# Kernel optimization log

Measured on AMD Instinct MI355X. Metric: run time of the kernel, lower is better.

The kernel has to match this reference:

```python
import jax, jax.numpy as jnp
import numpy as np

B = 4194304  # number of sequential rows


def setup_inputs() -> dict:
    key = jax.random.key(0)
    k1, k2, k3, k4 = jax.random.split(key, 4)
    x = jax.random.normal(k1, (B, 1, 3), dtype=jnp.float32)
    # nn.Linear(3, 3) params
    lim = 1.0 / np.sqrt(3.0)
    W = jax.random.uniform(k2, (3, 3), minval=-lim, maxval=lim, dtype=jnp.float32)
    b = jax.random.uniform(k3, (3,), minval=-lim, maxval=lim, dtype=jnp.float32)
    # FastNetwork init: (-1-1)*rand([3,1]) + 1  -> uniform in [-1, 1]
    net0 = jax.random.uniform(k4, (3, 1), minval=-1.0, maxval=1.0, dtype=jnp.float32)
    return {"x": x, "W": W, "b": b, "net0": net0}


def reference(x, W, b, net0):
    # x: [B,1,3]; W: [3,3]; b: [3]; net0: [3,1]
    xi = x[:, 0, :]                      # [B,3]
    # Updater: per-row Linear(3,3) -- batched as one matmul
    updates = xi @ W.T + b               # [B,3]

    def step(net, inp):
        x_row, u = inp                   # x_row: [3], u: [3]
        # 1/(1+exp(-10*(net + update - 0.5))) == sigmoid(10*(net + update - 0.5))
        net = jax.nn.sigmoid(10.0 * (net + u[:, None] - 0.5))  # [3,1]
        pred = x_row @ net               # [1]
        return net, pred

    _, preds = jax.lax.scan(step, net0, (xi, updates))
    return preds                         # [B,1]
```

## Files before the change

### kernel.cpp

```cpp
#include <hip/hip_runtime.h>


#if __has_builtin(__builtin_amdgcn_exp2f)
#define EXP2F(v) __builtin_amdgcn_exp2f(v)
#else
#define EXP2F(v) __expf(0.6931471805599453f * (v))
#endif

namespace {
constexpr int   BTOT   = 4194304;
constexpr int   CHUNK  = 16;
constexpr int   BLOCK  = 256;
constexpr int   BSTEPS = BLOCK * CHUNK;
constexpr int   WARM   = 32;
constexpr int   GRID   = BTOT / BSTEPS;
constexpr int   LDSF   = (BSTEPS + WARM) * 3;
constexpr float KEXP   = -14.426950408889634f;
constexpr float EPS    = 1e-6f;
}

#define CVALS(X0, X1, X2)                                                     \
  const float c0 = fmaf(kw00, (X0), fmaf(kw01, (X1), fmaf(kw02, (X2), kb0)));  \
  const float c1 = fmaf(kw10, (X0), fmaf(kw11, (X1), fmaf(kw12, (X2), kb1)));  \
  const float c2 = fmaf(kw20, (X0), fmaf(kw21, (X1), fmaf(kw22, (X2), kb2)));

#define SIG(N, C) __builtin_amdgcn_rcpf(1.0f + EXP2F(fmaf(KEXP, (N), (C))))

#define US(X0, X1, X2)                                                        \
  do {                                                                        \
    CVALS(X0, X1, X2)                                                         \
    lo0 = SIG(lo0, c0); hi0 = SIG(hi0, c0);                                   \
    lo1 = SIG(lo1, c1); hi1 = SIG(hi1, c1);                                   \
    lo2 = SIG(lo2, c2); hi2 = SIG(hi2, c2);                                   \
  } while (0)

#define SS(X0, X1, X2)                                                        \
  do {                                                                        \
    CVALS(X0, X1, X2)                                                         \
    m0 = SIG(m0, c0); m1 = SIG(m1, c1); m2 = SIG(m2, c2);                     \
  } while (0)

#define MS(IDX, X0, X1, X2)                                                   \
  do {                                                                        \
    CVALS(X0, X1, X2)                                                         \
    m0 = SIG(m0, c0); m1 = SIG(m1, c1); m2 = SIG(m2, c2);                     \
    pr[(IDX)] = fmaf((X0), m0, fmaf((X1), m1, (X2) * m2));                    \
  } while (0)

__global__ __launch_bounds__(BLOCK) void Updater_65395172049297_kernel(
    const float* __restrict__ x, const float* __restrict__ W,
    const float* __restrict__ bv, const float* __restrict__ n0v,
    float* __restrict__ out)
{
    __shared__ float lds[LDSF];

    const float kw00 = KEXP * W[0], kw01 = KEXP * W[1], kw02 = KEXP * W[2];
    const float kw10 = KEXP * W[3], kw11 = KEXP * W[4], kw12 = KEXP * W[5];
    const float kw20 = KEXP * W[6], kw21 = KEXP * W[7], kw22 = KEXP * W[8];
    const float kb0 = KEXP * (bv[0] - 0.5f);
    const float kb1 = KEXP * (bv[1] - 0.5f);
    const float kb2 = KEXP * (bv[2] - 0.5f);
    const float n00 = n0v[0], n01 = n0v[1], n02 = n0v[2];

    const long S = (long)blockIdx.x * BSTEPS;
    if (blockIdx.x == 0) {
        const float4* src = reinterpret_cast<const float4*>(x);
        float4*       dst = reinterpret_cast<float4*>(lds + WARM * 3);
        for (int i = threadIdx.x; i < BSTEPS * 3 / 4; i += BLOCK) dst[i] = src[i];
    } else {
        const float4* src = reinterpret_cast<const float4*>(x + 3 * (S - WARM));
        float4*       dst = reinterpret_cast<float4*>(lds);
        for (int i = threadIdx.x; i < LDSF / 4; i += BLOCK) dst[i] = src[i];
    }
    __syncthreads();

    const int  t     = threadIdx.x;
    const long start = S + (long)t * CHUNK;
    const int  wl    = (int)((start < (long)WARM) ? start : (long)WARM);
    const bool exact = (start - wl) == 0;
    const int  gw    = wl >> 2;
    const int  lbeg  = (int)(start - S + WARM) * 3 - wl * 3;

    float lo0, lo1, lo2, hi0, hi1, hi2, m0, m1, m2;
    bool  conv = false;
    int   g    = 0;

    if (exact) {
        m0 = n00; m1 = n01; m2 = n02; conv = true;
    } else {
        lo0 = lo1 = lo2 = 0.0f; hi0 = hi1 = hi2 = 1.0f;
        for (; g < gw; ) {
            const float4* p = reinterpret_cast<const float4*>(&lds[lbeg + 12 * g]);
            const float4 a = p[0], b4 = p[1], c4 = p[2];
            US(a.x, a.y, a.z);
            US(a.w, b4.x, b4.y);
            US(b4.z, b4.w, c4.x);
            US(c4.y, c4.z, c4.w);
            ++g;
            conv = ((hi0 - lo0) < EPS) & ((hi1 - lo1) < EPS) & ((hi2 - lo2) < EPS);
            if (__all(conv)) break;
        }
        if (conv) { m0 = 0.5f * (lo0 + hi0); m1 = 0.5f * (lo1 + hi1); m2 = 0.5f * (lo2 + hi2); }
    }

    if (conv) {
        for (; g < gw; ++g) {
            const float4* p = reinterpret_cast<const float4*>(&lds[lbeg + 12 * g]);
            const float4 a = p[0], b4 = p[1], c4 = p[2];
            SS(a.x, a.y, a.z);
            SS(a.w, b4.x, b4.y);
            SS(b4.z, b4.w, c4.x);
            SS(c4.y, c4.z, c4.w);
        }
    } else {
        for (int a = 1; a < 10 && !conv; ++a) {
            long wl2 = (long)WARM << (2 * a);
            long bgn = start - wl2;
            bool ex2 = (bgn <= 0);
            if (ex2) bgn = 0;
            if (ex2) { lo0 = hi0 = n00; lo1 = hi1 = n01; lo2 = hi2 = n02; }
            else     { lo0 = lo1 = lo2 = 0.0f; hi0 = hi1 = hi2 = 1.0f; }
            for (long s2 = bgn; s2 < start; ++s2) {
                const float X0 = x[3 * s2], X1 = x[3 * s2 + 1], X2 = x[3 * s2 + 2];
                US(X0, X1, X2);
            }
            conv = ex2 || (((hi0 - lo0) < EPS) & ((hi1 - lo1) < EPS) & ((hi2 - lo2) < EPS));
        }
        m0 = 0.5f * (lo0 + hi0); m1 = 0.5f * (lo1 + hi1); m2 = 0.5f * (lo2 + hi2);
    }

    const int lm = (int)(start - S + WARM) * 3;
    float pr[CHUNK];
#pragma unroll
    for (int q = 0; q < CHUNK / 4; ++q) {
        const float4* p = reinterpret_cast<const float4*>(&lds[lm + 12 * q]);
        const float4 a = p[0], b4 = p[1], c4 = p[2];
        MS(4 * q + 0, a.x, a.y, a.z);
        MS(4 * q + 1, a.w, b4.x, b4.y);
        MS(4 * q + 2, b4.z, b4.w, c4.x);
        MS(4 * q + 3, c4.y, c4.z, c4.w);
    }

    float4* op = reinterpret_cast<float4*>(out + start);
#pragma unroll
    for (int i = 0; i < CHUNK / 4; ++i)
        op[i] = make_float4(pr[4 * i + 0], pr[4 * i + 1], pr[4 * i + 2], pr[4 * i + 3]);
}

extern "C" void kernel_launch(void* const* d_in, const int* in_sizes, int n_in,
                              void* d_out, int out_size, void* d_ws, size_t ws_size,
                              hipStream_t stream) {
    const float* x   = (const float*)d_in[0];
    const float* W   = (const float*)d_in[1];
    const float* bv  = (const float*)d_in[2];
    const float* n0v = (const float*)d_in[3];
    float*       out = (float*)d_out;
    Updater_65395172049297_kernel<<<GRID, BLOCK, 0, stream>>>(x, W, bv, n0v, out);
}
```

Baseline: 101.6 us.

## Drop LDS staging and read inputs directly from global with prefetch

Removes the shared-memory staging buffer and its block-wide barrier. Each thread now reads its warm-up and main rows straight from global memory as float4, prefetching the next group during the warm-up loop. Launch bounds now request a minimum of 4 blocks per CU, and the fallback long warm-up loop is vectorised to float4. The trade-off is per-thread strided global reads (stride 48 bytes across lanes), which coalesce worse than the cooperative LDS copy but rely on cache hits and avoid LDS occupancy limits.

```diff
diff --git a/kernel.cpp b/kernel.cpp
--- a/kernel.cpp
+++ b/kernel.cpp
@@ -14,7 +14,6 @@
 constexpr int   BSTEPS = BLOCK * CHUNK;
 constexpr int   WARM   = 32;
 constexpr int   GRID   = BTOT / BSTEPS;
-constexpr int   LDSF   = (BSTEPS + WARM) * 3;
 constexpr float KEXP   = -14.426950408889634f;
 constexpr float EPS    = 1e-6f;
 }
@@ -47,13 +46,11 @@
     pr[(IDX)] = fmaf((X0), m0, fmaf((X1), m1, (X2) * m2));                    \
   } while (0)
 
-__global__ __launch_bounds__(BLOCK) void Updater_65395172049297_kernel(
+__global__ __launch_bounds__(BLOCK, 4) void Updater_65395172049297_kernel(
     const float* __restrict__ x, const float* __restrict__ W,
     const float* __restrict__ bv, const float* __restrict__ n0v,
     float* __restrict__ out)
 {
-    __shared__ float lds[LDSF];
-
     const float kw00 = KEXP * W[0], kw01 = KEXP * W[1], kw02 = KEXP * W[2];
     const float kw10 = KEXP * W[3], kw11 = KEXP * W[4], kw12 = KEXP * W[5];
     const float kw20 = KEXP * W[6], kw21 = KEXP * W[7], kw22 = KEXP * W[8];
@@ -62,24 +59,12 @@
     const float kb2 = KEXP * (bv[2] - 0.5f);
     const float n00 = n0v[0], n01 = n0v[1], n02 = n0v[2];
 
-    const long S = (long)blockIdx.x * BSTEPS;
-    if (blockIdx.x == 0) {
-        const float4* src = reinterpret_cast<const float4*>(x);
-        float4*       dst = reinterpret_cast<float4*>(lds + WARM * 3);
-        for (int i = threadIdx.x; i < BSTEPS * 3 / 4; i += BLOCK) dst[i] = src[i];
-    } else {
-        const float4* src = reinterpret_cast<const float4*>(x + 3 * (S - WARM));
-        float4*       dst = reinterpret_cast<float4*>(lds);
-        for (int i = threadIdx.x; i < LDSF / 4; i += BLOCK) dst[i] = src[i];
-    }
-    __syncthreads();
-
-    const int  t     = threadIdx.x;
-    const long start = S + (long)t * CHUNK;
+    const long start = (long)blockIdx.x * BSTEPS + (long)threadIdx.x * CHUNK;
     const int  wl    = (int)((start < (long)WARM) ? start : (long)WARM);
     const bool exact = (start - wl) == 0;
     const int  gw    = wl >> 2;
-    const int  lbeg  = (int)(start - S + WARM) * 3 - wl * 3;
+
+    const float4* wp = reinterpret_cast<const float4*>(x + 3 * (start - wl));
 
     float lo0, lo1, lo2, hi0, hi1, hi2, m0, m1, m2;
     bool  conv = false;
@@ -89,54 +74,58 @@
         m0 = n00; m1 = n01; m2 = n02; conv = true;
     } else {
         lo0 = lo1 = lo2 = 0.0f; hi0 = hi1 = hi2 = 1.0f;
-        for (; g < gw; ) {
-            const float4* p = reinterpret_cast<const float4*>(&lds[lbeg + 12 * g]);
-            const float4 a = p[0], b4 = p[1], c4 = p[2];
-            US(a.x, a.y, a.z);
-            US(a.w, b4.x, b4.y);
-            US(b4.z, b4.w, c4.x);
-            US(c4.y, c4.z, c4.w);
+        float4 A = wp[0], B4 = wp[1], C4 = wp[2];
+        while (g < gw) {
+            const float4 An = wp[3 * g + 3], Bn = wp[3 * g + 4], Cn = wp[3 * g + 5];
+            US(A.x, A.y, A.z);
+            US(A.w, B4.x, B4.y);
+            US(B4.z, B4.w, C4.x);
+            US(C4.y, C4.z, C4.w);
             ++g;
             conv = ((hi0 - lo0) < EPS) & ((hi1 - lo1) < EPS) & ((hi2 - lo2) < EPS);
             if (__all(conv)) break;
+            A = An; B4 = Bn; C4 = Cn;
         }
         if (conv) { m0 = 0.5f * (lo0 + hi0); m1 = 0.5f * (lo1 + hi1); m2 = 0.5f * (lo2 + hi2); }
     }
 
     if (conv) {
         for (; g < gw; ++g) {
-            const float4* p = reinterpret_cast<const float4*>(&lds[lbeg + 12 * g]);
-            const float4 a = p[0], b4 = p[1], c4 = p[2];
-            SS(a.x, a.y, a.z);
-            SS(a.w, b4.x, b4.y);
+            const float4 a4 = wp[3 * g], b4 = wp[3 * g + 1], c4 = wp[3 * g + 2];
+            SS(a4.x, a4.y, a4.z);
+            SS(a4.w, b4.x, b4.y);
             SS(b4.z, b4.w, c4.x);
             SS(c4.y, c4.z, c4.w);
         }
     } else {
-        for (int a = 1; a < 10 && !conv; ++a) {
-            long wl2 = (long)WARM << (2 * a);
+        for (int at = 1; at < 10 && !conv; ++at) {
+            long wl2 = (long)WARM << (2 * at);
             long bgn = start - wl2;
             bool ex2 = (bgn <= 0);
             if (ex2) bgn = 0;
             if (ex2) { lo0 = hi0 = n00; lo1 = hi1 = n01; lo2 = hi2 = n02; }
             else     { lo0 = lo1 = lo2 = 0.0f; hi0 = hi1 = hi2 = 1.0f; }
-            for (long s2 = bgn; s2 < start; ++s2) {
-                const float X0 = x[3 * s2], X1 = x[3 * s2 + 1], X2 = x[3 * s2 + 2];
-                US(X0, X1, X2);
+            const float4* bp = reinterpret_cast<const float4*>(x + 3 * bgn);
+            const long ng = (start - bgn) >> 2;
+            for (long q = 0; q < ng; ++q) {
+                const float4 a4 = bp[3 * q], b4 = bp[3 * q + 1], c4 = bp[3 * q + 2];
+                US(a4.x, a4.y, a4.z);
+                US(a4.w, b4.x, b4.y);
+                US(b4.z, b4.w, c4.x);
+                US(c4.y, c4.z, c4.w);
             }
             conv = ex2 || (((hi0 - lo0) < EPS) & ((hi1 - lo1) < EPS) & ((hi2 - lo2) < EPS));
         }
         m0 = 0.5f * (lo0 + hi0); m1 = 0.5f * (lo1 + hi1); m2 = 0.5f * (lo2 + hi2);
     }
 
-    const int lm = (int)(start - S + WARM) * 3;
+    const float4* mp = reinterpret_cast<const float4*>(x + 3 * start);
     float pr[CHUNK];
 #pragma unroll
     for (int q = 0; q < CHUNK / 4; ++q) {
-        const float4* p = reinterpret_cast<const float4*>(&lds[lm + 12 * q]);
-        const float4 a = p[0], b4 = p[1], c4 = p[2];
-        MS(4 * q + 0, a.x, a.y, a.z);
-        MS(4 * q + 1, a.w, b4.x, b4.y);
+        const float4 a4 = mp[3 * q], b4 = mp[3 * q + 1], c4 = mp[3 * q + 2];
+        MS(4 * q + 0, a4.x, a4.y, a4.z);
+        MS(4 * q + 1, a4.w, b4.x, b4.y);
         MS(4 * q + 2, b4.z, b4.w, c4.x);
         MS(4 * q + 3, c4.y, c4.z, c4.w);
     }
```

Result: slower. 117.4 us (+15.5%).
